# Kernel optimization log

Hardware: AMD Instinct MI355X
Metric: run time of the kernel (lower is better)

## Reference

```python
import jax, jax.numpy as jnp
import numpy as np

B = 64
E = 512          # latent_size / h_dim
H = 8            # num_heads
D = E // H       # head_dim
MAX_AGENTS = 254 # max(agents_per_sample) for the deterministic counts below
NEG = -1e9


def setup_inputs() -> dict:
    key = jax.random.key(0)
    k_x, k_wi, k_bi, k_wo, k_bo = jax.random.split(key, 5)
    # deterministic variable agent counts in [128, 254]; sum == 11531, max == 254
    agents = jnp.array([128 + (3 * i) % 129 for i in range(B)], dtype=jnp.int32)
    total = 11531
    att_in = jax.random.normal(k_x, (total, E), dtype=jnp.float32)
    # nn.MultiheadAttention params: packed in-proj [3E, E] + bias, out-proj [E, E] + bias
    w_in = jax.random.normal(k_wi, (3 * E, E), dtype=jnp.float32) * 0.02
    b_in = jax.random.normal(k_bi, (3 * E,), dtype=jnp.float32) * 0.02
    w_out = jax.random.normal(k_wo, (E, E), dtype=jnp.float32) * 0.02
    b_out = jax.random.normal(k_bo, (E,), dtype=jnp.float32) * 0.02
    return {"att_in": att_in, "w_in": w_in, "b_in": b_in,
            "w_out": w_out, "b_out": b_out, "agents_per_sample": agents}


def reference(att_in, w_in, b_in, w_out, b_out, agents_per_sample):
    S = MAX_AGENTS
    # scatter packed rows into padded [B, S, E] via a clipped gather (jit-safe)
    offsets = jnp.cumsum(agents_per_sample) - agents_per_sample      # [B]
    pos = jnp.arange(S, dtype=jnp.int32)
    mask = pos[None, :] < agents_per_sample[:, None]                 # [B, S] valid
    idx = jnp.clip(offsets[:, None] + pos[None, :], 0, att_in.shape[0] - 1)
    padded = jnp.where(mask[..., None], att_in[idx], 0.0)            # [B, S, E]

    # fused QKV projection (torch packed in_proj), dropout disabled (eval)
    qkv = padded @ w_in.T + b_in                                     # [B, S, 3E]
    q, k, v = jnp.split(qkv, 3, axis=-1)
    q = q.reshape(B, S, H, D)
    k = k.reshape(B, S, H, D)
    v = v.reshape(B, S, H, D)

    scores = jnp.einsum('bqhd,bkhd->bhqk', q, k) * (D ** -0.5)      # [B, H, S, S]
    scores = jnp.where(mask[:, None, None, :], scores, NEG)          # key_padding_mask
    attn = jax.nn.softmax(scores, axis=-1)
    ctx = jnp.einsum('bhqk,bkhd->bqhd', attn, v).reshape(B, S, E)
    out = ctx @ w_out.T + b_out                                      # [B, S, E]
    # torch returns only valid rows per sample; zero the padded rows instead
    return out * mask[..., None]
```

## Files before the change

kernel.cpp:

```cpp
#include <hip/hip_runtime.h>
#include <hip/hip_bf16.h>

typedef __attribute__((ext_vector_type(8))) short bf16x8;
typedef __attribute__((ext_vector_type(4))) float f32x4;
typedef __attribute__((ext_vector_type(4))) int i32x4;
typedef __attribute__((ext_vector_type(4))) unsigned short u16x4;
typedef __attribute__((ext_vector_type(2))) unsigned ui2;
typedef __attribute__((ext_vector_type(4))) float fl4;

struct __attribute__((packed)) u16x4u { u16x4 v; };

__device__ __forceinline__ f32x4 mfma16(bf16x8 a, bf16x8 b, f32x4 c) {
    return __builtin_amdgcn_mfma_f32_16x16x32_bf16(a, b, c, 0, 0, 0);
}

__device__ __forceinline__ unsigned short f2b(float f) {
    unsigned u = __float_as_uint(f);
    unsigned r = (u + 0x7FFF + ((u >> 16) & 1)) >> 16;
    return (unsigned short)r;
}

__device__ __forceinline__ int bsearch_off(const int* s_off, int m) {
    int lo = 0, hi = 63;
    while (lo < hi) {
        int mid = (lo + hi + 1) >> 1;
        if (s_off[mid] <= m) lo = mid; else hi = mid - 1;
    }
    return lo;
}

__device__ __forceinline__ void gld_lds16(const __hip_bfloat16* g, __hip_bfloat16* l) {
    __builtin_amdgcn_global_load_lds(
        (const __attribute__((address_space(1))) void*)g,
        (__attribute__((address_space(3))) void*)l,
        16, 0, 0);
}

__global__ void k_prep(const unsigned short* __restrict__ src,
                       const void* __restrict__ b_in, const void* __restrict__ b_out,
                       const int* __restrict__ agents,
                       int* __restrict__ flag, int* __restrict__ offs,
                       float* __restrict__ bfi, float* __restrict__ bfo) {
    __shared__ int sh[256];
    __shared__ int sa[64];
    __shared__ int sflag;
    int tid = threadIdx.x;
    int h = 0;
    for (int i = tid; i < 16384; i += 256) {
        unsigned e = (src[i] >> 7) & 0xFF;
        if (e == 0xFF) h = 1;
    }
    sh[tid] = h;
    if (tid < 64) sa[tid] = agents[tid];
    __syncthreads();
    if (tid == 0) {
        int any = 0;
        for (int i = 0; i < 256; ++i) any |= sh[i];
        flag[0] = any;
        sflag = any;
    }
    if (tid < 64) {
        int ex = 0;
        for (int i = 0; i < 64; ++i) { int v = sa[i]; if (i < tid) ex += v; }
        offs[tid] = ex;
        if (tid == 63) offs[64] = ex + sa[63];
    }
    __syncthreads();
    int f = sflag;
    for (int i = tid; i < 1536; i += 256)
        bfi[i] = f ? ((const float*)b_in)[i]
                   : __bfloat162float(((const __hip_bfloat16*)b_in)[i]);
    for (int i = tid; i < 512; i += 256)
        bfo[i] = f ? ((const float*)b_out)[i]
                   : __bfloat162float(((const __hip_bfloat16*)b_out)[i]);
}

__global__ void k_zero_pad(char* __restrict__ out, const int* __restrict__ agents,
                           const int* __restrict__ flag) {
    int b = blockIdx.x;
    int n = agents[b];
    int esz = flag[0] ? 4 : 2;
    long long base = ((long long)b * 254 + n) * 512 * esz;
    long long bytes = (long long)(254 - n) * 512 * esz;
    for (long long i = ((long long)blockIdx.y * 256 + threadIdx.x) * 16;
         i < bytes; i += (long long)8 * 256 * 16)
        *(i32x4*)(out + base + i) = (i32x4){0, 0, 0, 0};
}

__global__ void k_cast_all(const void* __restrict__ sA, unsigned short* __restrict__ dA, int nA,
                           const void* __restrict__ sWi, unsigned short* __restrict__ dWi, int nWi,
                           const void* __restrict__ sWo, unsigned short* __restrict__ dWo, int nWo,
                           const int* __restrict__ flag) {
    int i = (blockIdx.x * 256 + threadIdx.x) * 4;
    const void* src; unsigned short* dst; int k;
    if (i < nA)            { src = sA;  dst = dA;  k = i; }
    else if (i < nA + nWi) { src = sWi; dst = dWi; k = i - nA; }
    else if (i < nA + nWi + nWo) { src = sWo; dst = dWo; k = i - nA - nWi; }
    else return;
    u16x4 o;
    if (flag[0]) {
        fl4 v = *(const fl4*)((const float*)src + k);
        o[0] = f2b(v[0]); o[1] = f2b(v[1]); o[2] = f2b(v[2]); o[3] = f2b(v[3]);
    } else {
        o = *(const u16x4*)((const unsigned short*)src + k);
    }
    *(u16x4*)(dst + k) = o;
}

template<int LDA, bool MROWS>
__device__ __forceinline__ void gemm_core(
    const __hip_bfloat16* __restrict__ A,
    const __hip_bfloat16* __restrict__ W,
    int m0, int n0, int total,
    __hip_bfloat16* As, __hip_bfloat16* Ws,
    f32x4 acc[4][4], int tid)
{
    int lane = tid & 63, quad = lane >> 4, c = lane & 15;
    int wave = tid >> 6;
    int wr = wave >> 1, wc = wave & 1;

    const __hip_bfloat16* gA[4];
    const __hip_bfloat16* gW[4];
    __hip_bfloat16* lA[4];
    __hip_bfloat16* lW[4];
#pragma unroll
    for (int j = 0; j < 4; ++j) {
        int L = j * 256 + tid;
        int row = L >> 3;
        int gseg = (L & 7) ^ (row & 7);
        int ar = m0 + row; if (ar > total - 1) ar = total - 1;
        gA[j] = A + (size_t)ar * LDA + gseg * 8;
        gW[j] = W + (size_t)(n0 + row) * 512 + gseg * 8;
        lA[j] = As + (size_t)(j * 256 + wave * 64) * 8;
        lW[j] = Ws + (size_t)(j * 256 + wave * 64) * 8;
    }

#pragma unroll
    for (int j = 0; j < 4; ++j) gld_lds16(gA[j], lA[j]);
#pragma unroll
    for (int j = 0; j < 4; ++j) gld_lds16(gW[j], lW[j]);
    __syncthreads();

#pragma unroll
    for (int s = 0; s < 8; ++s) {
        const int cur = s & 1;
        const int nxt = cur ^ 1;
        if (s < 7) {
            int k0 = (s + 1) * 64;
#pragma unroll
            for (int j = 0; j < 4; ++j) gld_lds16(gA[j] + k0, lA[j] + nxt * (128 * 64));
#pragma unroll
            for (int j = 0; j < 4; ++j) gld_lds16(gW[j] + k0, lW[j] + nxt * (128 * 64));
        }
        const __hip_bfloat16* Ab = As + cur * (128 * 64);
        const __hip_bfloat16* Wb = Ws + cur * (128 * 64);
#pragma unroll
        for (int h = 0; h < 2; ++h) {
            bf16x8 af[4], wf[4];
#pragma unroll
            for (int t = 0; t < 4; ++t) {
                int rowa = wr * 64 + t * 16 + c;
                int rowb = wc * 64 + t * 16 + c;
                int ks = quad + 4 * h;
                af[t] = *(const bf16x8*)(Ab + (size_t)rowa * 64 + ((ks ^ (rowa & 7)) * 8));
                wf[t] = *(const bf16x8*)(Wb + (size_t)rowb * 64 + ((ks ^ (rowb & 7)) * 8));
            }
#pragma unroll
            for (int i = 0; i < 4; ++i)
#pragma unroll
                for (int j = 0; j < 4; ++j)
                    acc[i][j] = MROWS ? mfma16(af[i], wf[j], acc[i][j])
                                      : mfma16(wf[j], af[i], acc[i][j]);
        }
        if (s < 7) __syncthreads();
    }
}

__global__ __launch_bounds__(256) void k_qkv(
    const __hip_bfloat16* __restrict__ A,
    const __hip_bfloat16* __restrict__ W,
    const float* __restrict__ bias,
    const int* __restrict__ offs,
    __hip_bfloat16* __restrict__ qk,
    __hip_bfloat16* __restrict__ vT,
    int total, int MT)
{
    __shared__ __hip_bfloat16 As[2 * 128 * 64];
    __shared__ __hip_bfloat16 Ws[2 * 128 * 64];
    __shared__ int s_off[65];
    int l = blockIdx.x;
    int inner = l >> 3;
    int cb = inner % 12;
    int rb = (l & 7) + 8 * (inner / 12);
    if (rb >= MT) return;
    int n0 = cb * 128;
    int m0 = rb * 128;
    int tid = threadIdx.x;
    if (tid < 65) s_off[tid] = offs[tid];
    int lane = tid & 63, quad = lane >> 4, c = lane & 15;
    int wave = tid >> 6, wr = wave >> 1, wc = wave & 1;
    f32x4 z = {0.f, 0.f, 0.f, 0.f};
    f32x4 acc[4][4] = {{z,z,z,z},{z,z,z,z},{z,z,z,z},{z,z,z,z}};

    if (n0 < 1024) {
        gemm_core<512, false>(A, W, m0, n0, total, As, Ws, acc, tid);
        fl4 bv4[4];
#pragma unroll
        for (int j = 0; j < 4; ++j)
            bv4[j] = *(const fl4*)&bias[n0 + wc * 64 + j * 16 + quad * 4];
#pragma unroll
        for (int i = 0; i < 4; ++i) {
            int m = m0 + wr * 64 + i * 16 + c;
            if (m >= total) continue;
            size_t row = (size_t)m * 1024;
#pragma unroll
            for (int j = 0; j < 4; ++j) {
                int col0 = n0 + wc * 64 + j * 16 + quad * 4;
                u16x4 o;
#pragma unroll
                for (int r = 0; r < 4; ++r) o[r] = f2b(acc[i][j][r] + bv4[j][r]);
                *(u16x4*)&qk[row + col0] = o;
            }
        }
    } else {
        gemm_core<512, true>(A, W, m0, n0, total, As, Ws, acc, tid);
        float bv[4];
#pragma unroll
        for (int j = 0; j < 4; ++j) bv[j] = bias[n0 + wc * 64 + j * 16 + c];
#pragma unroll
        for (int i = 0; i < 4; ++i) {
            int m_base = m0 + wr * 64 + i * 16 + quad * 4;
            if (m_base >= total) continue;
            int lo = bsearch_off(s_off, m_base);
            bool vec = (m_base + 3 < total) && (s_off[lo + 1] > m_base + 3);
            if (vec) {
                int vs = m_base - s_off[lo];
#pragma unroll
                for (int j = 0; j < 4; ++j) {
                    int vc = n0 - 1024 + wc * 64 + j * 16 + c;
                    size_t idx = ((size_t)(lo * 8 + (vc >> 6)) * 64 + (vc & 63)) * 256 + vs;
                    u16x4 o;
#pragma unroll
                    for (int r = 0; r < 4; ++r) o[r] = f2b(acc[i][j][r] + bv[j]);
                    ((u16x4u*)&vT[idx])->v = o;
                }
            } else {
#pragma unroll
                for (int r = 0; r < 4; ++r) {
                    int m = m_base + r;
                    if (m >= total) continue;
                    int lo2 = bsearch_off(s_off, m);
                    int vs2 = m - s_off[lo2];
#pragma unroll
                    for (int j = 0; j < 4; ++j) {
                        int vc = n0 - 1024 + wc * 64 + j * 16 + c;
                        vT[((size_t)(lo2 * 8 + (vc >> 6)) * 64 + (vc & 63)) * 256 + vs2] =
                            __float2bfloat16(acc[i][j][r] + bv[j]);
                    }
                }
            }
        }
    }
}

__global__ __launch_bounds__(256, 2) void k_attn(
    __hip_bfloat16* __restrict__ qk,
    const __hip_bfloat16* __restrict__ vT,
    const int* __restrict__ agents,
    const int* __restrict__ offs)
{
    __shared__ __attribute__((aligned(16))) char Pl[4][16 * 80];
    int bh = blockIdx.x;
    int b = bh >> 3, h = bh & 7;
    int n = agents[b];
    int off = offs[b];
    int qtiles = (n + 15) >> 4;
    int stmax = (qtiles + 1) >> 1;
    int tid = threadIdx.x;
    int wave = tid >> 6, lane = tid & 63, quad = lane >> 4, c = lane & 15;
    const __hip_bfloat16* vbase = vT + (size_t)bh * 64 * 256;
    char* Plw = &Pl[wave][0];

    bf16x8 qB[4][2];
    int nt = 0;
#pragma unroll
    for (int t = 0; t < 4; ++t) {
        int qt = wave + 4 * t;
        if (qt < qtiles) {
            nt = t + 1;
            int qr = qt * 16 + c; if (qr > n - 1) qr = n - 1;
            const __hip_bfloat16* qp = qk + (size_t)(off + qr) * 1024 + h * 64 + quad * 8;
            qB[t][0] = *(const bf16x8*)qp;
            qB[t][1] = *(const bf16x8*)(qp + 32);
        }
    }

    f32x4 z = {0.f, 0.f, 0.f, 0.f};
    f32x4 O[4][4] = {{z,z,z,z},{z,z,z,z},{z,z,z,z},{z,z,z,z}};
    float sm[4] = {0.f, 0.f, 0.f, 0.f};
    const __hip_bfloat16* kg = qk + (size_t)off * 1024 + 512 + h * 64 + quad * 8;

    for (int st = 0; st < stmax; ++st) {
        int k0 = st * 32;
        bf16x8 kA[2][2];
#pragma unroll
        for (int ti = 0; ti < 2; ++ti) {
            int kr = k0 + ti * 16 + c; if (kr > n - 1) kr = n - 1;
            const __hip_bfloat16* kp = kg + (size_t)kr * 1024;
            kA[ti][0] = *(const bf16x8*)kp;
            kA[ti][1] = *(const bf16x8*)(kp + 32);
        }
        bf16x8 vA[4];
#pragma unroll
        for (int dt = 0; dt < 4; ++dt)
            vA[dt] = *(const bf16x8*)(vbase + (size_t)(dt * 16 + c) * 256 + k0 + quad * 8);

#pragma unroll
        for (int t = 0; t < 4; ++t) {
            if (t < nt) {
#pragma unroll
                for (int ti = 0; ti < 2; ++ti) {
                    f32x4 s = mfma16(kA[ti][0], qB[t][0], z);
                    s = mfma16(kA[ti][1], qB[t][1], s);
                    int kbase = k0 + ti * 16 + quad * 4;
                    float p0 = (kbase + 0 < n) ? __expf(s[0] * 0.125f) : 0.f;
                    float p1 = (kbase + 1 < n) ? __expf(s[1] * 0.125f) : 0.f;
                    float p2 = (kbase + 2 < n) ? __expf(s[2] * 0.125f) : 0.f;
                    float p3 = (kbase + 3 < n) ? __expf(s[3] * 0.125f) : 0.f;
                    sm[t] += (p0 + p1) + (p2 + p3);
                    ui2 dw;
                    dw[0] = (unsigned)f2b(p0) | ((unsigned)f2b(p1) << 16);
                    dw[1] = (unsigned)f2b(p2) | ((unsigned)f2b(p3) << 16);
                    *(ui2*)(Plw + c * 80 + ti * 32 + quad * 8) = dw;
                }
                bf16x8 pB = *(const bf16x8*)(Plw + c * 80 + quad * 16);
#pragma unroll
                for (int dt = 0; dt < 4; ++dt)
                    O[t][dt] = mfma16(vA[dt], pB, O[t][dt]);
            }
        }
    }

#pragma unroll
    for (int t = 0; t < 4; ++t) {
        if (t < nt) {
            float v = sm[t];
            v += __shfl_xor(v, 16);
            v += __shfl_xor(v, 32);
            float iv = 1.0f / v;
            int q = (wave + 4 * t) * 16 + c;
            if (q < n) {
                size_t row = (size_t)(off + q) * 1024 + h * 64;
#pragma unroll
                for (int dt = 0; dt < 4; ++dt) {
                    u16x4 o;
#pragma unroll
                    for (int r = 0; r < 4; ++r) o[r] = f2b(O[t][dt][r] * iv);
                    *(u16x4*)&qk[row + dt * 16 + quad * 4] = o;
                }
            }
        }
    }
}

__global__ __launch_bounds__(256) void k_out(
    const __hip_bfloat16* __restrict__ A,
    const __hip_bfloat16* __restrict__ W,
    const float* __restrict__ bias,
    const int* __restrict__ offs,
    void* __restrict__ out,
    const int* __restrict__ flag,
    int total, int MT)
{
    __shared__ __hip_bfloat16 As[2 * 128 * 64];
    __shared__ __hip_bfloat16 Ws[2 * 128 * 64];
    __shared__ int s_off[65];
    int l = blockIdx.x;
    int inner = l >> 3;
    int cb = inner & 3;
    int rb = (l & 7) + 8 * (inner >> 2);
    if (rb >= MT) return;
    int n0 = cb * 128;
    int m0 = rb * 128;
    int tid = threadIdx.x;
    if (tid < 65) s_off[tid] = offs[tid];
    f32x4 z = {0.f, 0.f, 0.f, 0.f};
    f32x4 acc[4][4] = {{z,z,z,z},{z,z,z,z},{z,z,z,z},{z,z,z,z}};
    gemm_core<1024, false>(A, W, m0, n0, total, As, Ws, acc, tid);

    int f32m = flag[0];
    int lane = tid & 63, quad = lane >> 4, c = lane & 15;
    int wave = tid >> 6, wr = wave >> 1, wc = wave & 1;
    fl4 bv4[4];
#pragma unroll
    for (int j = 0; j < 4; ++j)
        bv4[j] = *(const fl4*)&bias[n0 + wc * 64 + j * 16 + quad * 4];
#pragma unroll
    for (int i = 0; i < 4; ++i) {
        int m = m0 + wr * 64 + i * 16 + c;
        if (m >= total) continue;
        int lo = bsearch_off(s_off, m);
        int os_ = m - s_off[lo];
        size_t rowb = ((size_t)(lo * 254 + os_)) * 512;
#pragma unroll
        for (int j = 0; j < 4; ++j) {
            int col0 = n0 + wc * 64 + j * 16 + quad * 4;
            if (f32m) {
                fl4 o;
#pragma unroll
                for (int r = 0; r < 4; ++r) o[r] = acc[i][j][r] + bv4[j][r];
                *(fl4*)&((float*)out)[rowb + col0] = o;
            } else {
                u16x4 o;
#pragma unroll
                for (int r = 0; r < 4; ++r) o[r] = f2b(acc[i][j][r] + bv4[j][r]);
                *(u16x4*)&((__hip_bfloat16*)out)[rowb + col0] = o;
            }
        }
    }
}

extern "C" void kernel_launch(void* const* d_in, const int* in_sizes, int n_in,
                              void* d_out, int out_size, void* d_ws, size_t ws_size,
                              hipStream_t stream) {
    const void* att_in = d_in[0];
    const void* w_in   = d_in[1];
    const void* b_in   = d_in[2];
    const void* w_out  = d_in[3];
    const void* b_out  = d_in[4];
    const int* agents  = (const int*)d_in[5];
    int total = in_sizes[0] / 512;

    char* p = (char*)d_ws;
    int* flag  = (int*)p;                 p += 256;
    int* offs  = (int*)p;                 p += 512;
    float* bfi = (float*)p;               p += 1536 * 4;
    float* bfo = (float*)p;               p += 512 * 4;
    __hip_bfloat16* WinBf  = (__hip_bfloat16*)p;  p += (size_t)1536 * 512 * 2;
    __hip_bfloat16* WoutBf = (__hip_bfloat16*)p;  p += (size_t)512 * 512 * 2;
    __hip_bfloat16* Abf    = (__hip_bfloat16*)p;  p += (size_t)total * 512 * 2;
    __hip_bfloat16* qk     = (__hip_bfloat16*)p;  p += (size_t)total * 1024 * 2;
    __hip_bfloat16* vT     = (__hip_bfloat16*)p;  p += (size_t)64 * 8 * 64 * 256 * 2;

    int nA = total * 512, nWi = 1536 * 512, nWo = 512 * 512;
    int ntot = nA + nWi + nWo;

    k_prep<<<1, 256, 0, stream>>>((const unsigned short*)att_in, b_in, b_out,
                                  agents, flag, offs, bfi, bfo);
    k_zero_pad<<<dim3(64, 8), 256, 0, stream>>>((char*)d_out, agents, flag);
    k_cast_all<<<(ntot / 4 + 255) / 256, 256, 0, stream>>>(
        att_in, (unsigned short*)Abf, nA,
        w_in,   (unsigned short*)WinBf, nWi,
        w_out,  (unsigned short*)WoutBf, nWo, flag);

    int MT = (total + 127) / 128;
    int MTpad = ((MT + 7) / 8) * 8;
    k_qkv<<<12 * MTpad, 256, 0, stream>>>(Abf, WinBf, bfi, offs, qk, vT, total, MT);
    k_attn<<<512, 256, 0, stream>>>(qk, vT, agents, offs);
    k_out<<<4 * MTpad, 256, 0, stream>>>(qk, WoutBf, bfo, offs, d_out, flag, total, MT);
}
```

Baseline: 183.3 us.

## Split attention query tiles across two blocks and double-buffer K/V loads

The attention kernel now launches two blocks per (batch, head), each handling half the query tiles. This halves the per-block register state for Q and the accumulators, and the launch bound goes from 2 to 4 blocks per CU to raise occupancy. K and V fragments are software-pipelined with two register buffers, so the next step's global loads overlap the current step's MFMA work. The prep kernel's serial flag reduction is replaced with a ballot. The cost is that K/V get loaded twice, once per half-block, and the extra prefetch buffers raise register pressure.

Result: slower. 221.9 us (+21.1%).

```diff
diff --git a/kernel.cpp b/kernel.cpp
--- a/kernel.cpp
+++ b/kernel.cpp
@@ -53,15 +53,12 @@
     sh[tid] = h;
     if (tid < 64) sa[tid] = agents[tid];
     __syncthreads();
-    if (tid == 0) {
-        int any = 0;
-        for (int i = 0; i < 256; ++i) any |= sh[i];
-        flag[0] = any;
-        sflag = any;
-    }
     if (tid < 64) {
+        int v = sh[tid] | sh[tid + 64] | sh[tid + 128] | sh[tid + 192];
+        unsigned long long m = __ballot(v != 0);
+        if (tid == 0) { flag[0] = (m != 0) ? 1 : 0; sflag = (m != 0) ? 1 : 0; }
         int ex = 0;
-        for (int i = 0; i < 64; ++i) { int v = sa[i]; if (i < tid) ex += v; }
+        for (int i = 0; i < 64; ++i) { int w = sa[i]; if (i < tid) ex += w; }
         offs[tid] = ex;
         if (tid == 63) offs[64] = ex + sa[63];
     }
@@ -263,29 +260,31 @@
     }
 }
 
-__global__ __launch_bounds__(256, 2) void k_attn(
+__global__ __launch_bounds__(256, 4) void k_attn(
     __hip_bfloat16* __restrict__ qk,
     const __hip_bfloat16* __restrict__ vT,
     const int* __restrict__ agents,
     const int* __restrict__ offs)
 {
     __shared__ __attribute__((aligned(16))) char Pl[4][16 * 80];
-    int bh = blockIdx.x;
+    int bid = blockIdx.x;
+    int bh = bid >> 1, part = bid & 1;
     int b = bh >> 3, h = bh & 7;
     int n = agents[b];
     int off = offs[b];
     int qtiles = (n + 15) >> 4;
+    if (part * 8 >= qtiles) return;
     int stmax = (qtiles + 1) >> 1;
     int tid = threadIdx.x;
     int wave = tid >> 6, lane = tid & 63, quad = lane >> 4, c = lane & 15;
     const __hip_bfloat16* vbase = vT + (size_t)bh * 64 * 256;
     char* Plw = &Pl[wave][0];
 
-    bf16x8 qB[4][2];
+    bf16x8 qB[2][2];
     int nt = 0;
 #pragma unroll
-    for (int t = 0; t < 4; ++t) {
-        int qt = wave + 4 * t;
+    for (int t = 0; t < 2; ++t) {
+        int qt = part * 8 + wave + 4 * t;
         if (qt < qtiles) {
             nt = t + 1;
             int qr = qt * 16 + c; if (qr > n - 1) qr = n - 1;
@@ -296,13 +295,12 @@
     }
 
     f32x4 z = {0.f, 0.f, 0.f, 0.f};
-    f32x4 O[4][4] = {{z,z,z,z},{z,z,z,z},{z,z,z,z},{z,z,z,z}};
-    float sm[4] = {0.f, 0.f, 0.f, 0.f};
+    f32x4 O[2][4] = {{z,z,z,z},{z,z,z,z}};
+    float sm[2] = {0.f, 0.f};
     const __hip_bfloat16* kg = qk + (size_t)off * 1024 + 512 + h * 64 + quad * 8;
 
-    for (int st = 0; st < stmax; ++st) {
+    auto LK = [&](int st, bf16x8 kA[2][2], bf16x8 vA[4]) {
         int k0 = st * 32;
-        bf16x8 kA[2][2];
 #pragma unroll
         for (int ti = 0; ti < 2; ++ti) {
             int kr = k0 + ti * 16 + c; if (kr > n - 1) kr = n - 1;
@@ -310,13 +308,15 @@
             kA[ti][0] = *(const bf16x8*)kp;
             kA[ti][1] = *(const bf16x8*)(kp + 32);
         }
-        bf16x8 vA[4];
 #pragma unroll
         for (int dt = 0; dt < 4; ++dt)
             vA[dt] = *(const bf16x8*)(vbase + (size_t)(dt * 16 + c) * 256 + k0 + quad * 8);
-
-#pragma unroll
-        for (int t = 0; t < 4; ++t) {
+    };
+
+    auto CMP = [&](int st, bf16x8 kA[2][2], bf16x8 vA[4]) {
+        int k0 = st * 32;
+#pragma unroll
+        for (int t = 0; t < 2; ++t) {
             if (t < nt) {
 #pragma unroll
                 for (int ti = 0; ti < 2; ++ti) {
@@ -339,16 +339,27 @@
                     O[t][dt] = mfma16(vA[dt], pB, O[t][dt]);
             }
         }
-    }
-
-#pragma unroll
-    for (int t = 0; t < 4; ++t) {
+    };
+
+    bf16x8 kA[2][2], vA[4], kB[2][2], vB[4];
+    LK(0, kA, vA);
+    for (int st = 0; st < stmax; st += 2) {
+        if (st + 1 < stmax) LK(st + 1, kB, vB);
+        CMP(st, kA, vA);
+        if (st + 1 < stmax) {
+            if (st + 2 < stmax) LK(st + 2, kA, vA);
+            CMP(st + 1, kB, vB);
+        }
+    }
+
+#pragma unroll
+    for (int t = 0; t < 2; ++t) {
         if (t < nt) {
             float v = sm[t];
             v += __shfl_xor(v, 16);
             v += __shfl_xor(v, 32);
             float iv = 1.0f / v;
-            int q = (wave + 4 * t) * 16 + c;
+            int q = (part * 8 + wave + 4 * t) * 16 + c;
             if (q < n) {
                 size_t row = (size_t)(off + q) * 1024 + h * 64;
 #pragma unroll
@@ -456,6 +467,6 @@
     int MT = (total + 127) / 128;
     int MTpad = ((MT + 7) / 8) * 8;
     k_qkv<<<12 * MTpad, 256, 0, stream>>>(Abf, WinBf, bfi, offs, qk, vT, total, MT);
-    k_attn<<<512, 256, 0, stream>>>(qk, vT, agents, offs);
+    k_attn<<<1024, 256, 0, stream>>>(qk, vT, agents, offs);
     k_out<<<4 * MTpad, 256, 0, stream>>>(qk, WoutBf, bfo, offs, d_out, flag, total, MT);
 }
```
